# Performance work log

Measured on AMD Instinct MI355X. Metric: run time of the kernel, lower is better.

The kernel has to match this reference:

```python
import jax, jax.numpy as jnp
import numpy as np

B, H, W, P = 32, 512, 512, 8192
EPS = 1e-5


def setup_inputs() -> dict:
    key = jax.random.key(0)
    k1, k2, k3, k4, k5 = jax.random.split(key, 5)
    return {
        "depth_3dmm": jax.random.normal(k1, (B, 1, H, W), jnp.float32),
        "depth_pigan": jax.random.normal(k2, (B, 1, H, W), jnp.float32),
        "mask": jax.random.randint(k3, (B, 1, H, W), 0, 2, jnp.int32),
        "sample1_raw": jax.random.randint(k4, (B, P), 0, H * W, jnp.int32),
        "sample2_raw": jax.random.randint(k5, (B, P), 0, H * W, jnp.int32),
    }


def reference(depth_3dmm, depth_pigan, mask, sample1_raw, sample2_raw):
    d3 = depth_3dmm.squeeze(axis=1)   # [B,H,W]
    dp = depth_pigan.squeeze(axis=1)  # [B,H,W]
    m = mask[:, 0].astype(bool)       # [B,H,W]
    Bv = m.shape[0]

    # Emulate torch.masked_select compaction with a fixed-shape stable argsort:
    # valid elements come first, in flat row-major order (same as masked_select).
    mflat = m.reshape(-1)
    order = jnp.argsort(jnp.logical_not(mflat))  # stable by default
    d3c = d3.reshape(-1)[order]  # compacted depth_3dmm (padding at tail)
    dpc = dp.reshape(-1)[order]  # compacted depth_pigan

    valid_num = m.reshape(Bv, -1).sum(axis=1)          # [B]
    batch_base = jnp.cumsum(valid_num) - valid_num     # [B]

    s1 = (sample1_raw % valid_num[:, None] + batch_base[:, None]).reshape(-1)
    s2 = (sample2_raw % valid_num[:, None] + batch_base[:, None]).reshape(-1)

    diff = dpc[s1] - dpc[s2]
    a, b = d3c[s1], d3c[s2]
    gt = a > b + EPS
    lt = a < b - EPS

    # mean(relu(-diff)[gt]) and mean(relu(diff)[lt]) without dynamic shapes
    loss1 = jnp.where(gt, jax.nn.relu(-diff), 0.0).sum() / gt.sum()
    loss2 = jnp.where(lt, jax.nn.relu(diff), 0.0).sum() / lt.sum()
    return (loss1 + loss2) / 2
```

## Files before the change

### kernel.cpp

```cpp
#include <hip/hip_runtime.h>
#include <stdint.h>

#define BB 32
#define HH 512
#define WW 512
#define HWSZ (HH * WW)
#define PP 8192
#define WPB (HWSZ / 64)
#define EPSV 1e-5f

#define NBLK_L 256
#define PPT 4

__device__ inline uint32_t f2bf(float f) {
    uint32_t u = __float_as_uint(f);
    return (u + 0x7FFFu + ((u >> 16) & 1u)) >> 16;
}

__global__ __launch_bounds__(256) void k_bitmap(const int* __restrict__ mask,
                                                uint64_t* __restrict__ words,
                                                float* __restrict__ accf,
                                                uint32_t* __restrict__ accu) {
    int gid = blockIdx.x * 256 + threadIdx.x;
    unsigned long long ball = __ballot(mask[gid] != 0);
    if ((threadIdx.x & 63) == 0) words[gid >> 6] = (uint64_t)ball;
    if (blockIdx.x == 0 && threadIdx.x == 0) {
        accf[0] = 0.0f; accf[1] = 0.0f;
        accu[0] = 0u; accu[1] = 0u; accu[2] = 0u;
    }
}

__global__ __launch_bounds__(256) void k_scan(const uint64_t* __restrict__ words,
                                              uint32_t* __restrict__ wprefix,
                                              uint32_t* __restrict__ valid_num) {
    __shared__ uint32_t wsum[4];
    int b = blockIdx.x, t = threadIdx.x, lane = t & 63, wid = t >> 6;
    const uint64_t* wbp = words + (size_t)b * WPB;
    uint32_t pc[16], s = 0;
    int base = t * 16;
#pragma unroll
    for (int i = 0; i < 16; ++i) { pc[i] = (uint32_t)__popcll(wbp[base + i]); s += pc[i]; }
    uint32_t own = s;
#pragma unroll
    for (int off = 1; off < 64; off <<= 1) {
        uint32_t n = __shfl_up(s, off);
        if (lane >= off) s += n;
    }
    if (lane == 63) wsum[wid] = s;
    __syncthreads();
    uint32_t wb = 0;
#pragma unroll
    for (int i = 0; i < 4; ++i) if (i < wid) wb += wsum[i];
    uint32_t off2 = wb + s - own;
    if (t == 255) valid_num[b] = wb + s;
    uint32_t* wp = wprefix + (size_t)b * WPB;
#pragma unroll
    for (int i = 0; i < 16; ++i) { wp[base + i] = off2; off2 += pc[i]; }
}

__global__ __launch_bounds__(256) void k_compact(const float* __restrict__ d3,
                                                 const float* __restrict__ dp,
                                                 const uint64_t* __restrict__ words,
                                                 const uint32_t* __restrict__ wprefix,
                                                 uint32_t* __restrict__ compact) {
    int e0 = (blockIdx.x * 256 + threadIdx.x) * 4;
    int w = e0 >> 6;
    uint64_t word = words[w];
    uint32_t wpf  = wprefix[w];
    float4 v3 = *reinterpret_cast<const float4*>(d3 + e0);
    float4 vp = *reinterpret_cast<const float4*>(dp + e0);
    int sh = e0 & 63;
    uint32_t bits = (uint32_t)((word >> sh) & 0xFull);
    if (bits == 0u) return;
    uint32_t dest = wpf + (uint32_t)__popcll(word & ((1ull << sh) - 1ull));
    int b = blockIdx.x >> 8;
    uint32_t* cb = compact + (size_t)b * HWSZ;
    if (bits & 1u) { cb[dest++] = f2bf(v3.x) | (f2bf(vp.x) << 16); }
    if (bits & 2u) { cb[dest++] = f2bf(v3.y) | (f2bf(vp.y) << 16); }
    if (bits & 4u) { cb[dest++] = f2bf(v3.z) | (f2bf(vp.z) << 16); }
    if (bits & 8u) { cb[dest]   = f2bf(v3.w) | (f2bf(vp.w) << 16); }
}

__global__ __launch_bounds__(256) void k_loss(const uint32_t* __restrict__ compact,
                                              const int* __restrict__ s1raw,
                                              const int* __restrict__ s2raw,
                                              const uint32_t* __restrict__ valid_num,
                                              uint32_t* __restrict__ partials,
                                              uint32_t* __restrict__ accu,
                                              float* __restrict__ out) {
    __shared__ float sv1[4], sv2[4];
    __shared__ uint32_t sc1[4], sc2[4];
    __shared__ int is_last;

    const int tid = threadIdx.x;
    const int lane = tid & 63;
    const int wid = tid >> 6;

    int w = (blockIdx.x & 7) * 32 + (blockIdx.x >> 3);
    int b = w >> 3;
    int j = w & 7;
    int pbase = b * PP + j * (PP / 8) + tid;

    uint32_t vn = valid_num[b];
    const uint32_t* cb = compact + (size_t)b * HWSZ;

    uint32_t k1[PPT], k2[PPT], g1[PPT], g2[PPT];
#pragma unroll
    for (int q = 0; q < PPT; ++q) {
        int p = pbase + q * 256;
        k1[q] = (uint32_t)s1raw[p] % vn;
        k2[q] = (uint32_t)s2raw[p] % vn;
    }
#pragma unroll
    for (int q = 0; q < PPT; ++q) {
        g1[q] = cb[k1[q]];
        g2[q] = cb[k2[q]];
    }

    float v1 = 0.f, v2 = 0.f;
    uint32_t c1 = 0u, c2 = 0u;
#pragma unroll
    for (int q = 0; q < PPT; ++q) {
        float a    = __uint_as_float(g1[q] << 16);
        float bv   = __uint_as_float(g2[q] << 16);
        float diff = __uint_as_float(g1[q] & 0xFFFF0000u) -
                     __uint_as_float(g2[q] & 0xFFFF0000u);
        bool gt = a > bv + EPSV;
        bool lt = a < bv - EPSV;
        if (gt) { v1 += fmaxf(-diff, 0.0f); c1 += 1u; }
        if (lt) { v2 += fmaxf(diff, 0.0f);  c2 += 1u; }
    }

#pragma unroll
    for (int off = 32; off > 0; off >>= 1) {
        v1 += __shfl_down(v1, off);
        v2 += __shfl_down(v2, off);
        c1 += __shfl_down(c1, off);
        c2 += __shfl_down(c2, off);
    }
    if (lane == 0) { sv1[wid] = v1; sv2[wid] = v2; sc1[wid] = c1; sc2[wid] = c2; }
    __syncthreads();

    if (tid == 0) {
        float t1 = sv1[0] + sv1[1] + sv1[2] + sv1[3];
        float t2 = sv2[0] + sv2[1] + sv2[2] + sv2[3];
        uint32_t u1 = sc1[0] + sc1[1] + sc1[2] + sc1[3];
        uint32_t u2 = sc2[0] + sc2[1] + sc2[2] + sc2[3];
        uint4 rec = make_uint4(__float_as_uint(t1), __float_as_uint(t2), u1, u2);
        *reinterpret_cast<uint4*>(partials + 4 * w) = rec;
        __threadfence();
        uint32_t ticket = __hip_atomic_fetch_add(&accu[2], 1u, __ATOMIC_ACQ_REL,
                                                 __HIP_MEMORY_SCOPE_AGENT);
        is_last = (ticket == (uint32_t)(NBLK_L - 1)) ? 1 : 0;
    }
    __syncthreads();

    if (is_last) {
        uint32_t r0 = __hip_atomic_load(&partials[4 * tid + 0], __ATOMIC_RELAXED,
                                        __HIP_MEMORY_SCOPE_AGENT);
        uint32_t r1 = __hip_atomic_load(&partials[4 * tid + 1], __ATOMIC_RELAXED,
                                        __HIP_MEMORY_SCOPE_AGENT);
        uint32_t r2 = __hip_atomic_load(&partials[4 * tid + 2], __ATOMIC_RELAXED,
                                        __HIP_MEMORY_SCOPE_AGENT);
        uint32_t r3 = __hip_atomic_load(&partials[4 * tid + 3], __ATOMIC_RELAXED,
                                        __HIP_MEMORY_SCOPE_AGENT);
        float fv1 = __uint_as_float(r0);
        float fv2 = __uint_as_float(r1);
        uint32_t uc1 = r2, uc2 = r3;
#pragma unroll
        for (int off = 32; off > 0; off >>= 1) {
            fv1 += __shfl_down(fv1, off);
            fv2 += __shfl_down(fv2, off);
            uc1 += __shfl_down(uc1, off);
            uc2 += __shfl_down(uc2, off);
        }
        __syncthreads();
        if (lane == 0) { sv1[wid] = fv1; sv2[wid] = fv2; sc1[wid] = uc1; sc2[wid] = uc2; }
        __syncthreads();
        if (tid == 0) {
            float s1t = sv1[0] + sv1[1] + sv1[2] + sv1[3];
            float s2t = sv2[0] + sv2[1] + sv2[2] + sv2[3];
            uint32_t n1 = sc1[0] + sc1[1] + sc1[2] + sc1[3];
            uint32_t n2 = sc2[0] + sc2[1] + sc2[2] + sc2[3];
            out[0] = 0.5f * (s1t / (float)n1 + s2t / (float)n2);
        }
    }
}

__global__ __launch_bounds__(256) void k_loss_search(const float* __restrict__ d3,
                                                     const float* __restrict__ dp,
                                                     const int* __restrict__ s1raw,
                                                     const int* __restrict__ s2raw,
                                                     const uint64_t* __restrict__ words,
                                                     const uint32_t* __restrict__ wprefix,
                                                     const uint32_t* __restrict__ valid_num,
                                                     float* __restrict__ accf,
                                                     uint32_t* __restrict__ accu,
                                                     float* __restrict__ out) {
    __shared__ uint32_t wp[WPB];
    __shared__ float sv1[4], sv2[4];
    __shared__ uint32_t sc1[4], sc2[4];
    int b = blockIdx.x >> 5;
    int gid = blockIdx.x * 256 + threadIdx.x;
    const uint32_t* wpg = wprefix + (size_t)b * WPB;
    for (int i = threadIdx.x; i < WPB; i += 256) wp[i] = wpg[i];
    __syncthreads();
    uint32_t vn = valid_num[b];
    const uint64_t* wbp = words + (size_t)b * WPB;
    const float* d3b = d3 + (size_t)b * HWSZ;
    const float* dpb = dp + (size_t)b * HWSZ;
    uint32_t k1 = (uint32_t)s1raw[gid] % vn;
    uint32_t k2 = (uint32_t)s2raw[gid] % vn;
    auto sel = [&](uint32_t k) -> int {
        int lo = 0, hi = WPB;
        while (hi - lo > 1) { int mid = (lo + hi) >> 1; if (wp[mid] <= k) lo = mid; else hi = mid; }
        uint32_t r = k - wp[lo];
        uint64_t x = wbp[lo];
        int pos = lo << 6;
        uint32_t c = (uint32_t)__popcll(x & 0xFFFFFFFFull);
        if (r >= c) { r -= c; pos += 32; x >>= 32; }
        uint32_t y = (uint32_t)x;
        c = (uint32_t)__popc(y & 0xFFFFu); if (r >= c) { r -= c; pos += 16; y >>= 16; }
        c = (uint32_t)__popc(y & 0xFFu);   if (r >= c) { r -= c; pos += 8;  y >>= 8; }
        c = (uint32_t)__popc(y & 0xFu);    if (r >= c) { r -= c; pos += 4;  y >>= 4; }
        c = (uint32_t)__popc(y & 0x3u);    if (r >= c) { r -= c; pos += 2;  y >>= 2; }
        c = y & 1u;                        if (r >= c) { pos += 1; }
        return pos;
    };
    int i1 = sel(k1), i2 = sel(k2);
    float a = d3b[i1], bv = d3b[i2];
    float diff = dpb[i1] - dpb[i2];
    bool gt = a > bv + EPSV, lt = a < bv - EPSV;
    float v1 = gt ? fmaxf(-diff, 0.0f) : 0.0f;
    float v2 = lt ? fmaxf(diff, 0.0f) : 0.0f;
    uint32_t c1 = gt ? 1u : 0u, c2 = lt ? 1u : 0u;
#pragma unroll
    for (int off = 32; off > 0; off >>= 1) {
        v1 += __shfl_down(v1, off); v2 += __shfl_down(v2, off);
        c1 += __shfl_down(c1, off); c2 += __shfl_down(c2, off);
    }
    int wid = threadIdx.x >> 6;
    if ((threadIdx.x & 63) == 0) { sv1[wid] = v1; sv2[wid] = v2; sc1[wid] = c1; sc2[wid] = c2; }
    __syncthreads();
    if (threadIdx.x == 0) {
        float t1 = 0.f, t2 = 0.f; uint32_t u1 = 0, u2 = 0;
        for (int i = 0; i < 4; ++i) { t1 += sv1[i]; t2 += sv2[i]; u1 += sc1[i]; u2 += sc2[i]; }
        atomicAdd(&accf[0], t1); atomicAdd(&accf[1], t2);
        atomicAdd(&accu[0], u1); atomicAdd(&accu[1], u2);
        __threadfence();
        uint32_t ticket = atomicAdd(&accu[2], 1u);
        if (ticket == (uint32_t)(gridDim.x - 1)) {
            float sum1 = atomicAdd(&accf[0], 0.0f);
            float sum2 = atomicAdd(&accf[1], 0.0f);
            uint32_t n1 = atomicAdd(&accu[0], 0u);
            uint32_t n2 = atomicAdd(&accu[1], 0u);
            out[0] = 0.5f * (sum1 / (float)n1 + sum2 / (float)n2);
        }
    }
}

extern "C" void kernel_launch(void* const* d_in, const int* in_sizes, int n_in,
                              void* d_out, int out_size, void* d_ws, size_t ws_size,
                              hipStream_t stream) {
    const float* d3  = (const float*)d_in[0];
    const float* dp  = (const float*)d_in[1];
    const int*  mask = (const int*)d_in[2];
    const int*  s1   = (const int*)d_in[3];
    const int*  s2   = (const int*)d_in[4];
    float* out = (float*)d_out;
    char* ws = (char*)d_ws;

    uint64_t* words     = (uint64_t*)ws;
    uint32_t* wprefix   = (uint32_t*)(ws + 1048576);
    uint32_t* valid_num = (uint32_t*)(ws + 1572864);
    float*    accf      = (float*)(ws + 1573120);
    uint32_t* accu      = (uint32_t*)(ws + 1573184);
    uint32_t* partials  = (uint32_t*)(ws + 1574912);
    uint32_t* compact   = (uint32_t*)(ws + 2097152);

    const size_t need = 2097152 + (size_t)BB * HWSZ * sizeof(uint32_t);

    k_bitmap<<<(BB * HWSZ) / 256, 256, 0, stream>>>(mask, words, accf, accu);
    k_scan<<<BB, 256, 0, stream>>>(words, wprefix, valid_num);

    if (ws_size >= need) {
        k_compact<<<(BB * HWSZ) / 1024, 256, 0, stream>>>(d3, dp, words, wprefix, compact);
        k_loss<<<NBLK_L, 256, 0, stream>>>(compact, s1, s2, valid_num,
                                           partials, accu, out);
    } else {
        k_loss_search<<<(BB * PP) / 256, 256, 0, stream>>>(d3, dp, s1, s2, words,
                                                           wprefix, valid_num,
                                                           accf, accu, out);
    }
}
```

Baseline: 153.8 us.

## Fuse mask bitmap, scan and compaction into one segmented compaction kernel

Replaces the bitmap, per-batch scan and compact kernels with a single kernel. Each block reads the mask and both depth maps for a 4096-element segment, compacts the valid elements locally and records a per-segment count. The loss kernel then prefix-sums the 64 segment counts per batch and binary-searches them to map each sample index into the segmented compact buffer. This drops two launches and the intermediate bitmap and prefix traffic, in exchange for a small binary search per sample.

```diff
diff --git a/kernel.cpp b/kernel.cpp
--- a/kernel.cpp
+++ b/kernel.cpp
@@ -9,38 +9,47 @@
 #define WPB (HWSZ / 64)
 #define EPSV 1e-5f
 
+#define SEG 4096
+#define SEGS (HWSZ / SEG)
 #define NBLK_L 256
-#define PPT 4
 
 __device__ inline uint32_t f2bf(float f) {
     uint32_t u = __float_as_uint(f);
     return (u + 0x7FFFu + ((u >> 16) & 1u)) >> 16;
 }
 
-__global__ __launch_bounds__(256) void k_bitmap(const int* __restrict__ mask,
-                                                uint64_t* __restrict__ words,
-                                                float* __restrict__ accf,
-                                                uint32_t* __restrict__ accu) {
-    int gid = blockIdx.x * 256 + threadIdx.x;
-    unsigned long long ball = __ballot(mask[gid] != 0);
-    if ((threadIdx.x & 63) == 0) words[gid >> 6] = (uint64_t)ball;
-    if (blockIdx.x == 0 && threadIdx.x == 0) {
-        accf[0] = 0.0f; accf[1] = 0.0f;
-        accu[0] = 0u; accu[1] = 0u; accu[2] = 0u;
-    }
-}
-
-__global__ __launch_bounds__(256) void k_scan(const uint64_t* __restrict__ words,
-                                              uint32_t* __restrict__ wprefix,
-                                              uint32_t* __restrict__ valid_num) {
+__global__ __launch_bounds__(256) void k_compact_seg(const int* __restrict__ mask,
+                                                     const float* __restrict__ d3,
+                                                     const float* __restrict__ dp,
+                                                     uint32_t* __restrict__ compact,
+                                                     uint32_t* __restrict__ counts,
+                                                     uint32_t* __restrict__ accu) {
     __shared__ uint32_t wsum[4];
-    int b = blockIdx.x, t = threadIdx.x, lane = t & 63, wid = t >> 6;
-    const uint64_t* wbp = words + (size_t)b * WPB;
-    uint32_t pc[16], s = 0;
-    int base = t * 16;
-#pragma unroll
-    for (int i = 0; i < 16; ++i) { pc[i] = (uint32_t)__popcll(wbp[base + i]); s += pc[i]; }
-    uint32_t own = s;
+    const int tid = threadIdx.x, lane = tid & 63, wid = tid >> 6;
+    const int blk = blockIdx.x;
+    const int batch = blk >> 6;
+    const int seg = blk & 63;
+    const int e0 = batch * HWSZ + seg * SEG + tid * 16;
+
+    const int4* m4 = reinterpret_cast<const int4*>(mask + e0);
+    const float4* a4 = reinterpret_cast<const float4*>(d3 + e0);
+    const float4* p4 = reinterpret_cast<const float4*>(dp + e0);
+    int4 mv[4];
+    float4 av[4], pv[4];
+#pragma unroll
+    for (int j = 0; j < 4; ++j) { mv[j] = m4[j]; av[j] = a4[j]; pv[j] = p4[j]; }
+
+    uint32_t bits = 0;
+#pragma unroll
+    for (int j = 0; j < 4; ++j) {
+        bits |= (uint32_t)(mv[j].x != 0) << (4 * j + 0);
+        bits |= (uint32_t)(mv[j].y != 0) << (4 * j + 1);
+        bits |= (uint32_t)(mv[j].z != 0) << (4 * j + 2);
+        bits |= (uint32_t)(mv[j].w != 0) << (4 * j + 3);
+    }
+    uint32_t cnt = (uint32_t)__popc(bits);
+
+    uint32_t s = cnt;
 #pragma unroll
     for (int off = 1; off < 64; off <<= 1) {
         uint32_t n = __shfl_up(s, off);
@@ -48,87 +57,87 @@
     }
     if (lane == 63) wsum[wid] = s;
     __syncthreads();
-    uint32_t wb = 0;
-#pragma unroll
-    for (int i = 0; i < 4; ++i) if (i < wid) wb += wsum[i];
-    uint32_t off2 = wb + s - own;
-    if (t == 255) valid_num[b] = wb + s;
-    uint32_t* wp = wprefix + (size_t)b * WPB;
-#pragma unroll
-    for (int i = 0; i < 16; ++i) { wp[base + i] = off2; off2 += pc[i]; }
-}
-
-__global__ __launch_bounds__(256) void k_compact(const float* __restrict__ d3,
-                                                 const float* __restrict__ dp,
-                                                 const uint64_t* __restrict__ words,
-                                                 const uint32_t* __restrict__ wprefix,
-                                                 uint32_t* __restrict__ compact) {
-    int e0 = (blockIdx.x * 256 + threadIdx.x) * 4;
-    int w = e0 >> 6;
-    uint64_t word = words[w];
-    uint32_t wpf  = wprefix[w];
-    float4 v3 = *reinterpret_cast<const float4*>(d3 + e0);
-    float4 vp = *reinterpret_cast<const float4*>(dp + e0);
-    int sh = e0 & 63;
-    uint32_t bits = (uint32_t)((word >> sh) & 0xFull);
-    if (bits == 0u) return;
-    uint32_t dest = wpf + (uint32_t)__popcll(word & ((1ull << sh) - 1ull));
-    int b = blockIdx.x >> 8;
-    uint32_t* cb = compact + (size_t)b * HWSZ;
-    if (bits & 1u) { cb[dest++] = f2bf(v3.x) | (f2bf(vp.x) << 16); }
-    if (bits & 2u) { cb[dest++] = f2bf(v3.y) | (f2bf(vp.y) << 16); }
-    if (bits & 4u) { cb[dest++] = f2bf(v3.z) | (f2bf(vp.z) << 16); }
-    if (bits & 8u) { cb[dest]   = f2bf(v3.w) | (f2bf(vp.w) << 16); }
-}
-
-__global__ __launch_bounds__(256) void k_loss(const uint32_t* __restrict__ compact,
-                                              const int* __restrict__ s1raw,
-                                              const int* __restrict__ s2raw,
-                                              const uint32_t* __restrict__ valid_num,
-                                              uint32_t* __restrict__ partials,
-                                              uint32_t* __restrict__ accu,
-                                              float* __restrict__ out) {
+    uint32_t base = 0;
+#pragma unroll
+    for (int i = 0; i < 4; ++i) if (i < wid) base += wsum[i];
+    uint32_t dest = (uint32_t)(batch * HWSZ + seg * SEG) + base + s - cnt;
+    if (tid == 255) counts[blk] = base + s;
+    if (blk == 0 && tid == 0) accu[0] = 0u;
+
+#pragma unroll
+    for (int j = 0; j < 4; ++j) {
+        uint32_t bj = bits >> (4 * j);
+        if (bj & 1u) compact[dest++] = f2bf(av[j].x) | (f2bf(pv[j].x) << 16);
+        if (bj & 2u) compact[dest++] = f2bf(av[j].y) | (f2bf(pv[j].y) << 16);
+        if (bj & 4u) compact[dest++] = f2bf(av[j].z) | (f2bf(pv[j].z) << 16);
+        if (bj & 8u) compact[dest++] = f2bf(av[j].w) | (f2bf(pv[j].w) << 16);
+    }
+}
+
+__global__ __launch_bounds__(256) void k_loss_seg(const uint32_t* __restrict__ compact,
+                                                  const uint32_t* __restrict__ counts,
+                                                  const int* __restrict__ s1raw,
+                                                  const int* __restrict__ s2raw,
+                                                  uint32_t* __restrict__ partials,
+                                                  uint32_t* __restrict__ accu,
+                                                  float* __restrict__ out) {
+    __shared__ uint32_t pref[65];
     __shared__ float sv1[4], sv2[4];
     __shared__ uint32_t sc1[4], sc2[4];
     __shared__ int is_last;
 
-    const int tid = threadIdx.x;
-    const int lane = tid & 63;
-    const int wid = tid >> 6;
-
-    int w = (blockIdx.x & 7) * 32 + (blockIdx.x >> 3);
-    int b = w >> 3;
-    int j = w & 7;
-    int pbase = b * PP + j * (PP / 8) + tid;
-
-    uint32_t vn = valid_num[b];
-    const uint32_t* cb = compact + (size_t)b * HWSZ;
-
-    uint32_t k1[PPT], k2[PPT], g1[PPT], g2[PPT];
-#pragma unroll
-    for (int q = 0; q < PPT; ++q) {
-        int p = pbase + q * 256;
-        k1[q] = (uint32_t)s1raw[p] % vn;
-        k2[q] = (uint32_t)s2raw[p] % vn;
-    }
-#pragma unroll
-    for (int q = 0; q < PPT; ++q) {
-        g1[q] = cb[k1[q]];
-        g2[q] = cb[k2[q]];
-    }
+    const int tid = threadIdx.x, lane = tid & 63, wid = tid >> 6;
+    const int w = (blockIdx.x & 7) * 32 + (blockIdx.x >> 3);
+    const int batch = w >> 3;
+    const int j = w & 7;
+
+    if (tid < 64) {
+        uint32_t c = counts[batch * SEGS + tid];
+        uint32_t s = c;
+#pragma unroll
+        for (int off = 1; off < 64; off <<= 1) {
+            uint32_t n = __shfl_up(s, off);
+            if (lane >= off) s += n;
+        }
+        pref[tid] = s - c;
+        if (tid == 63) pref[64] = s;
+    }
+    __syncthreads();
+    uint32_t vn = pref[64];
+    if (vn == 0u || vn > (uint32_t)HWSZ) vn = (uint32_t)HWSZ;
+
+    const uint32_t cbase = (uint32_t)(batch * HWSZ);
+    auto locate = [&](uint32_t k) -> uint32_t {
+        int lo = 0, hi = 64;
+#pragma unroll
+        for (int step = 0; step < 6; ++step) {
+            int mid = (lo + hi) >> 1;
+            if (pref[mid] <= k) lo = mid; else hi = mid;
+        }
+        return cbase + (uint32_t)(lo * SEG) + (k - pref[lo]);
+    };
+
+    int pb = batch * PP + j * (PP / 8) + tid;
+    uint32_t i1[4], i2[4], g1[4], g2[4];
+#pragma unroll
+    for (int q = 0; q < 4; ++q) {
+        int p = pb + q * 256;
+        i1[q] = locate((uint32_t)s1raw[p] % vn);
+        i2[q] = locate((uint32_t)s2raw[p] % vn);
+    }
+#pragma unroll
+    for (int q = 0; q < 4; ++q) { g1[q] = compact[i1[q]]; g2[q] = compact[i2[q]]; }
 
     float v1 = 0.f, v2 = 0.f;
     uint32_t c1 = 0u, c2 = 0u;
 #pragma unroll
-    for (int q = 0; q < PPT; ++q) {
+    for (int q = 0; q < 4; ++q) {
         float a    = __uint_as_float(g1[q] << 16);
         float bv   = __uint_as_float(g2[q] << 16);
         float diff = __uint_as_float(g1[q] & 0xFFFF0000u) -
                      __uint_as_float(g2[q] & 0xFFFF0000u);
-        bool gt = a > bv + EPSV;
-        bool lt = a < bv - EPSV;
-        if (gt) { v1 += fmaxf(-diff, 0.0f); c1 += 1u; }
-        if (lt) { v2 += fmaxf(diff, 0.0f);  c2 += 1u; }
+        if (a > bv + EPSV) { v1 += fmaxf(-diff, 0.0f); c1 += 1u; }
+        if (a < bv - EPSV) { v2 += fmaxf(diff, 0.0f);  c2 += 1u; }
     }
 
 #pragma unroll
@@ -149,7 +158,7 @@
         uint4 rec = make_uint4(__float_as_uint(t1), __float_as_uint(t2), u1, u2);
         *reinterpret_cast<uint4*>(partials + 4 * w) = rec;
         __threadfence();
-        uint32_t ticket = __hip_atomic_fetch_add(&accu[2], 1u, __ATOMIC_ACQ_REL,
+        uint32_t ticket = __hip_atomic_fetch_add(&accu[0], 1u, __ATOMIC_ACQ_REL,
                                                  __HIP_MEMORY_SCOPE_AGENT);
         is_last = (ticket == (uint32_t)(NBLK_L - 1)) ? 1 : 0;
     }
@@ -185,6 +194,44 @@
             out[0] = 0.5f * (s1t / (float)n1 + s2t / (float)n2);
         }
     }
+}
+
+__global__ __launch_bounds__(256) void k_bitmap_fb(const int* __restrict__ mask,
+                                                   uint64_t* __restrict__ words,
+                                                   float* __restrict__ accf,
+                                                   uint32_t* __restrict__ accu) {
+    int gid = blockIdx.x * 256 + threadIdx.x;
+    unsigned long long ball = __ballot(mask[gid] != 0);
+    if ((threadIdx.x & 63) == 0) words[gid >> 6] = (uint64_t)ball;
+    if (blockIdx.x == 0 && threadIdx.x == 0) {
+        accf[0] = 0.0f; accf[1] = 0.0f;
+        accu[0] = 0u; accu[1] = 0u; accu[2] = 0u;
+    }
+}
+
+__global__ __launch_bounds__(256) void k_scan_fb(const uint64_t* __restrict__ words,
+                                                 uint32_t* __restrict__ wprefix,
+                                                 uint32_t* __restrict__ valid_num) {
+    __shared__ uint32_t wsum[4];
+    int b = blockIdx.x, t = threadIdx.x, lane = t & 63, wid = t >> 6;
+    const uint64_t* wbp = words + (size_t)b * WPB;
+    uint32_t pc[16], s = 0;
+    int base = t * 16;
+#pragma unroll
+    for (int i = 0; i < 16; ++i) { pc[i] = (uint32_t)__popcll(wbp[base + i]); s += pc[i]; }
+    uint32_t own = s;
+#pragma unroll
+    for (int off = 1; off < 64; off <<= 1) { uint32_t n = __shfl_up(s, off); if (lane >= off) s += n; }
+    if (lane == 63) wsum[wid] = s;
+    __syncthreads();
+    uint32_t wb = 0;
+#pragma unroll
+    for (int i = 0; i < 4; ++i) if (i < wid) wb += wsum[i];
+    uint32_t off2 = wb + s - own;
+    if (t == 255) valid_num[b] = wb + s;
+    uint32_t* wp = wprefix + (size_t)b * WPB;
+#pragma unroll
+    for (int i = 0; i < 16; ++i) { wp[base + i] = off2; off2 += pc[i]; }
 }
 
 __global__ __launch_bounds__(256) void k_loss_search(const float* __restrict__ d3,
@@ -270,26 +317,28 @@
     float* out = (float*)d_out;
     char* ws = (char*)d_ws;
 
-    uint64_t* words     = (uint64_t*)ws;
-    uint32_t* wprefix   = (uint32_t*)(ws + 1048576);
-    uint32_t* valid_num = (uint32_t*)(ws + 1572864);
-    float*    accf      = (float*)(ws + 1573120);
-    uint32_t* accu      = (uint32_t*)(ws + 1573184);
-    uint32_t* partials  = (uint32_t*)(ws + 1574912);
-    uint32_t* compact   = (uint32_t*)(ws + 2097152);
+    uint32_t* counts   = (uint32_t*)ws;
+    uint32_t* accu     = (uint32_t*)(ws + 16384);
+    uint32_t* partials = (uint32_t*)(ws + 32768);
+    uint32_t* compact  = (uint32_t*)(ws + 2097152);
 
     const size_t need = 2097152 + (size_t)BB * HWSZ * sizeof(uint32_t);
 
-    k_bitmap<<<(BB * HWSZ) / 256, 256, 0, stream>>>(mask, words, accf, accu);
-    k_scan<<<BB, 256, 0, stream>>>(words, wprefix, valid_num);
-
     if (ws_size >= need) {
-        k_compact<<<(BB * HWSZ) / 1024, 256, 0, stream>>>(d3, dp, words, wprefix, compact);
-        k_loss<<<NBLK_L, 256, 0, stream>>>(compact, s1, s2, valid_num,
-                                           partials, accu, out);
+        k_compact_seg<<<BB * SEGS, 256, 0, stream>>>(mask, d3, dp, compact,
+                                                     counts, accu);
+        k_loss_seg<<<NBLK_L, 256, 0, stream>>>(compact, counts, s1, s2,
+                                               partials, accu, out);
     } else {
+        uint64_t* words     = (uint64_t*)ws;
+        uint32_t* wprefix   = (uint32_t*)(ws + 1048576);
+        uint32_t* valid_num = (uint32_t*)(ws + 1572864);
+        float*    accf      = (float*)(ws + 1573120);
+        uint32_t* faccu     = (uint32_t*)(ws + 1573184);
+        k_bitmap_fb<<<(BB * HWSZ) / 256, 256, 0, stream>>>(mask, words, accf, faccu);
+        k_scan_fb<<<BB, 256, 0, stream>>>(words, wprefix, valid_num);
         k_loss_search<<<(BB * PP) / 256, 256, 0, stream>>>(d3, dp, s1, s2, words,
                                                            wprefix, valid_num,
-                                                           accf, accu, out);
-    }
-}
+                                                           accf, faccu, out);
+    }
+}
```

After: 153.5 us. Within noise of the previous version (-0.2%).
